# Performance work log

Hardware: AMD Instinct MI355X
Metric: run time of the kernel (lower is better)

The kernel has to match this reference:

```python
import jax, jax.numpy as jnp
import numpy as np

N = 50000
E = 800000
IN_F = 128
OUT_F = 128


def setup_inputs() -> dict:
    key = jax.random.key(0)
    k1, k2, k3, k4, k5 = jax.random.split(key, 5)
    x = jax.random.normal(k1, (N, IN_F), dtype=jnp.float32)
    # sparse adjacency as COO edge list: row = dst (aggregating node), col = src
    edge_index = jax.random.randint(k2, (2, E), 0, N, dtype=jnp.int64)
    edge_weight = jax.random.uniform(k3, (E,), dtype=jnp.float32)
    # nn.Linear(in_features, out_features): W is [out, in], b is [out]
    W = jax.random.normal(k4, (OUT_F, IN_F), dtype=jnp.float32) * (1.0 / np.sqrt(IN_F))
    b = jax.random.normal(k5, (OUT_F,), dtype=jnp.float32) * 0.01
    return {"x": x, "edge_index": edge_index, "edge_weight": edge_weight, "W": W, "b": b}


def reference(x, edge_index, edge_weight, W, b):
    # hidden = self.linear(x)  -> [N, out]
    hidden = jnp.einsum("ni,oi->no", x, W) + b
    # out = adj @ hidden (SpMM): out[dst] += w_e * hidden[src]
    dst = edge_index[0]
    src = edge_index[1]
    msgs = edge_weight[:, None] * hidden[src]  # [E, out]
    out = jax.ops.segment_sum(msgs, dst, num_segments=x.shape[0])
    return out
```

## Files before the change

kernel.cpp:

```cpp
#include <hip/hip_runtime.h>
#include <hip/hip_bf16.h>

#define N_NODES 50000
#define N_EDGES 800000
#define FEAT    128
#define N_TILES (N_NODES / 16)
#define GEMM_BLOCKS 784
#define MAXD    32
#define OVF_CAP 16384
#define NODES_PER_GRP 6250
#define CHUNK   2048
#define NCHUNK  ((N_EDGES + CHUNK - 1) / CHUNK)
#define QCAP    110000
#define SCAT_BPG 98

using short8  = __attribute__((ext_vector_type(8))) short;
using float4v = __attribute__((ext_vector_type(4))) float;


__device__ __forceinline__ unsigned short f2b(float f) {
    __hip_bfloat16 h = __float2bfloat16(f);
    return __builtin_bit_cast(unsigned short, h);
}

__global__ __launch_bounds__(256) void k_prep(const float* __restrict__ W,
                                              int* __restrict__ ws_ints,
                                              unsigned short* __restrict__ wbf) {
    const int gid = blockIdx.x * 256 + threadIdx.x;
    if (gid < 12576) ((int4*)ws_ints)[gid] = make_int4(0, 0, 0, 0);
    if (gid < 2048) {
        const float* s = W + (size_t)gid * 8;
        float4v a0 = *(const float4v*)(s);
        float4v a1 = *(const float4v*)(s + 4);
        short8 v;
        #pragma unroll
        for (int j = 0; j < 4; ++j) { v[j] = (short)f2b(a0[j]); v[4 + j] = (short)f2b(a1[j]); }
        *(short8*)(wbf + (size_t)gid * 8) = v;
    }
}

__global__ __launch_bounds__(256) void k_fused(const float* __restrict__ x,
                                               const unsigned short* __restrict__ wbf,
                                               const float* __restrict__ bias,
                                               unsigned short* __restrict__ hidden,
                                               const int* __restrict__ ei,
                                               const float* __restrict__ wt,
                                               int* __restrict__ flag,
                                               int2* __restrict__ queue) {
    __shared__ int pshared[16];
    const int t = threadIdx.x;

    if (blockIdx.x < GEMM_BLOCKS) {
        const int wave = t >> 6;
        const int lane = t & 63;
        int tile = blockIdx.x * 4 + wave;
        if (tile >= N_TILES) tile = N_TILES - 1;
        const int rowBase = tile * 16;
        const int m    = lane & 15;
        const int quad = lane >> 4;

        float4v acc[8];
        #pragma unroll
        for (int i = 0; i < 8; ++i) acc[i] = (float4v){0.f, 0.f, 0.f, 0.f};

        short8 af[4];
        #pragma unroll
        for (int kk = 0; kk < 4; ++kk) {
            const int k0 = kk * 32 + quad * 8;
            const float* ap = x + (size_t)(rowBase + m) * FEAT + k0;
            float4v a0 = *(const float4v*)(ap);
            float4v a1 = *(const float4v*)(ap + 4);
            #pragma unroll
            for (int j = 0; j < 4; ++j) { af[kk][j] = (short)f2b(a0[j]); af[kk][4 + j] = (short)f2b(a1[j]); }
        }

        #pragma unroll
        for (int nt = 0; nt < 8; ++nt) {
            const unsigned short* wrow = wbf + (size_t)(nt * 16 + m) * FEAT + quad * 8;
            #pragma unroll
            for (int kk = 0; kk < 4; ++kk) {
                short8 bf = *(const short8*)(wrow + kk * 32);
                acc[nt] = __builtin_amdgcn_mfma_f32_16x16x32_bf16(af[kk], bf, acc[nt], 0, 0, 0);
            }
        }

        const int r0 = rowBase + quad * 4;
        #pragma unroll
        for (int nt = 0; nt < 8; ++nt) {
            const int col = nt * 16 + m;
            const float bc = bias[col];
            #pragma unroll
            for (int r = 0; r < 4; ++r) {
                hidden[(size_t)(r0 + r) * FEAT + col] = f2b(acc[nt][r] + bc);
            }
        }
    } else {
        int* lcnt  = pshared;
        int* gbase = pshared + 8;
        const int bid  = blockIdx.x - GEMM_BLOCKS;
        const int lane = t & 63;

        unsigned long long mball = __ballot(ei[2 * lane + 1] != 0);
        const int sh = (mball == 0ULL) ? 1 : 0;

        if (t < 8) lcnt[t] = 0;
        __syncthreads();

        const int e0 = bid * CHUNK + t;
        int      dstv[8];
        unsigned recv_[8];
        int      lpos[8];
        #pragma unroll
        for (int i = 0; i < 8; ++i) {
            int e = e0 + i * 256;
            if (e < N_EDGES) {
                int dst = ei[(size_t)e << sh];
                if ((unsigned)dst >= N_NODES) dst = 0;
                int src = ei[(size_t)(N_EDGES + e) << sh];
                if ((unsigned)src >= N_NODES) src = 0;
                dstv[i]  = dst;
                recv_[i] = ((unsigned)f2b(wt[e]) << 16) | (unsigned)src;
                lpos[i]  = atomicAdd(&lcnt[dst / NODES_PER_GRP], 1);
            } else {
                dstv[i] = -1;
            }
        }
        __syncthreads();
        if (t < 8) gbase[t] = atomicAdd(&flag[16 + 16 * t], lcnt[t]);
        __syncthreads();

        #pragma unroll
        for (int i = 0; i < 8; ++i) {
            if (dstv[i] < 0) continue;
            int g   = dstv[i] / NODES_PER_GRP;
            int idx = gbase[g] + lpos[i];
            if (idx < QCAP) {
                int2 r; r.x = dstv[i]; r.y = (int)recv_[i];
                queue[(size_t)g * QCAP + idx] = r;
            }
        }
    }
}

__global__ __launch_bounds__(256) void k_scat(const int2* __restrict__ queue,
                                              int* __restrict__ flag,
                                              int* __restrict__ fill,
                                              unsigned int* __restrict__ slots,
                                              int2* __restrict__ ovf) {
    const int g = blockIdx.x & 7;
    const int b = blockIdx.x >> 3;
    int n = flag[16 + 16 * g]; if (n > QCAP) n = QCAP;
    const int2* q = queue + (size_t)g * QCAP;

    for (int i = b * 256 + (int)threadIdx.x; i < n; i += SCAT_BPG * 256) {
        int2 ent = q[i];
        int dst = ent.x;
        int pos = atomicAdd(&fill[dst], 1);
        if (pos < MAXD) {
            slots[(size_t)dst * MAXD + pos] = (unsigned int)ent.y;
        } else {
            int op = atomicAdd(&flag[1], 1);
            if (op < OVF_CAP) { int2 r; r.x = dst; r.y = ent.y; ovf[op] = r; }
        }
    }
}

#define AGG_FMA(w_, h_)                                                      \
    acc[0] = fmaf(w_, __uint_as_float((h_.x & 0xffffu) << 16), acc[0]);      \
    acc[1] = fmaf(w_, __uint_as_float(h_.x & 0xffff0000u),     acc[1]);      \
    acc[2] = fmaf(w_, __uint_as_float((h_.y & 0xffffu) << 16), acc[2]);      \
    acc[3] = fmaf(w_, __uint_as_float(h_.y & 0xffff0000u),     acc[3]);      \
    acc[4] = fmaf(w_, __uint_as_float((h_.z & 0xffffu) << 16), acc[4]);      \
    acc[5] = fmaf(w_, __uint_as_float(h_.z & 0xffff0000u),     acc[5]);      \
    acc[6] = fmaf(w_, __uint_as_float((h_.w & 0xffffu) << 16), acc[6]);      \
    acc[7] = fmaf(w_, __uint_as_float(h_.w & 0xffff0000u),     acc[7]);

__global__ __launch_bounds__(256) void k_agg(const int* __restrict__ fill,
                                             const unsigned int* __restrict__ slots,
                                             const unsigned int* __restrict__ hid,
                                             const int* __restrict__ flag,
                                             const int2* __restrict__ ovf,
                                             float* __restrict__ out) {
    const int wave = threadIdx.x >> 6;
    const int lane = threadIdx.x & 63;
    const int node = blockIdx.x * 4 + wave;
    const int grp  = lane >> 4;
    const int sub  = lane & 15;

    const int degf = fill[node];
    const int deg  = (degf > MAXD) ? MAXD : degf;
    const uint4* sl4 = (const uint4*)(slots + (size_t)node * MAXD);

    float acc[8];
    #pragma unroll
    for (int j = 0; j < 8; ++j) acc[j] = 0.f;

    const int iters = (deg + 3) >> 2;
    for (int it = 0; it < iters; it += 4) {
        uint4 r0 = sl4[it];
        uint4 r1 = sl4[(it + 1) & 7];
        uint4 r2 = sl4[(it + 2) & 7];
        uint4 r3 = sl4[(it + 3) & 7];
        unsigned rc0 = (grp < 2) ? (grp == 0 ? r0.x : r0.y) : (grp == 2 ? r0.z : r0.w);
        unsigned rc1 = (grp < 2) ? (grp == 0 ? r1.x : r1.y) : (grp == 2 ? r1.z : r1.w);
        unsigned rc2 = (grp < 2) ? (grp == 0 ? r2.x : r2.y) : (grp == 2 ? r2.z : r2.w);
        unsigned rc3 = (grp < 2) ? (grp == 0 ? r3.x : r3.y) : (grp == 2 ? r3.z : r3.w);
        const int e0 = it * 4 + grp;
        const bool v0 = (e0)      < deg;
        const bool v1 = (e0 + 4)  < deg;
        const bool v2 = (e0 + 8)  < deg;
        const bool v3 = (e0 + 12) < deg;
        const float w0 = v0 ? __uint_as_float(rc0 & 0xffff0000u) : 0.f;
        const float w1 = v1 ? __uint_as_float(rc1 & 0xffff0000u) : 0.f;
        const float w2 = v2 ? __uint_as_float(rc2 & 0xffff0000u) : 0.f;
        const float w3 = v3 ? __uint_as_float(rc3 & 0xffff0000u) : 0.f;
        const unsigned s0 = v0 ? (rc0 & 0xffffu) : 0u;
        const unsigned s1 = v1 ? (rc1 & 0xffffu) : 0u;
        const unsigned s2 = v2 ? (rc2 & 0xffffu) : 0u;
        const unsigned s3 = v3 ? (rc3 & 0xffffu) : 0u;
        uint4 h0 = *((const uint4*)(hid + (size_t)s0 * 64) + sub);
        uint4 h1 = *((const uint4*)(hid + (size_t)s1 * 64) + sub);
        uint4 h2 = *((const uint4*)(hid + (size_t)s2 * 64) + sub);
        uint4 h3 = *((const uint4*)(hid + (size_t)s3 * 64) + sub);
        AGG_FMA(w0, h0)
        AGG_FMA(w1, h1)
        AGG_FMA(w2, h2)
        AGG_FMA(w3, h3)
    }

    if (degf > MAXD) {
        int n = flag[1]; if (n > OVF_CAP) n = OVF_CAP;
        for (int i = 0; i < n; ++i) {
            int2 r = ovf[i];
            if (r.x != node || (i & 3) != grp) continue;
            unsigned rec = (unsigned)r.y;
            float w = __uint_as_float(rec & 0xffff0000u);
            unsigned src = rec & 0xffffu;
            uint4 h = *((const uint4*)(hid + (size_t)src * 64) + sub);
            AGG_FMA(w, h)
        }
    }

    #pragma unroll
    for (int j = 0; j < 8; ++j) {
        float a = acc[j];
        a += __shfl_xor(a, 16, 64);
        a += __shfl_xor(a, 32, 64);
        acc[j] = a;
    }

    if (lane < 16) {
        float* o = out + (size_t)node * FEAT + sub * 8;
        *(float4*)(o)     = make_float4(acc[0], acc[1], acc[2], acc[3]);
        *(float4*)(o + 4) = make_float4(acc[4], acc[5], acc[6], acc[7]);
    }
}

extern "C" void kernel_launch(void* const* d_in, const int* in_sizes, int n_in,
                              void* d_out, int out_size, void* d_ws, size_t ws_size,
                              hipStream_t stream) {
    const float* x  = (const float*)d_in[0];
    const int*   ei = (const int*)d_in[1];
    const float* ew = (const float*)d_in[2];
    const float* W  = (const float*)d_in[3];
    const float* b  = (const float*)d_in[4];
    float* out = (float*)d_out;

    int*  flag = (int*)d_ws;
    int*  fill = flag + 256;
    int2* ovf  = (int2*)(fill + 50048);
    unsigned int* slots = (unsigned int*)(ovf + OVF_CAP);
    unsigned short* hidden = (unsigned short*)(slots + (size_t)N_NODES * MAXD);
    int2* queue = (int2*)(hidden + (size_t)N_NODES * FEAT);
    unsigned short* wbf = (unsigned short*)(queue + (size_t)8 * QCAP);

    k_prep <<<64, 256, 0, stream>>>(W, flag, wbf);
    k_fused<<<GEMM_BLOCKS + NCHUNK, 256, 0, stream>>>(x, wbf, b, hidden, ei, ew,
                                                      flag, queue);
    k_scat <<<8 * SCAT_BPG, 256, 0, stream>>>(queue, flag, fill, slots, ovf);
    k_agg  <<<N_NODES / 4, 256, 0, stream>>>(fill, slots, (const unsigned int*)hidden,
                                             flag, ovf, out);
}
```

Before: 178.2 us.

## Stage swizzled bf16 W in LDS for GEMM and batch scatter atomics

The prep kernel now writes the bf16 weight matrix in an XOR-swizzled layout. Each GEMM block copies the whole matrix into a 32KB shared-memory buffer and reads B fragments from LDS without bank conflicts, instead of reloading them from global memory per wave. The scatter kernel is unrolled by four so several queue loads and fill atomics are in flight at once. The large shared allocation now also applies to the partition blocks, which may lower occupancy there. The added LDS staging and barrier could also cost more than the cached global reads saved.

```diff
diff --git a/kernel.cpp b/kernel.cpp
--- a/kernel.cpp
+++ b/kernel.cpp
@@ -29,13 +29,16 @@
     const int gid = blockIdx.x * 256 + threadIdx.x;
     if (gid < 12576) ((int4*)ws_ints)[gid] = make_int4(0, 0, 0, 0);
     if (gid < 2048) {
-        const float* s = W + (size_t)gid * 8;
+        const int r  = gid >> 4;
+        const int cc = gid & 15;
+        const float* s = W + (size_t)r * FEAT + cc * 8;
         float4v a0 = *(const float4v*)(s);
         float4v a1 = *(const float4v*)(s + 4);
         short8 v;
         #pragma unroll
         for (int j = 0; j < 4; ++j) { v[j] = (short)f2b(a0[j]); v[4 + j] = (short)f2b(a1[j]); }
-        *(short8*)(wbf + (size_t)gid * 8) = v;
+        const int dst = r * 16 + (cc ^ (r & 7));
+        *(short8*)(wbf + (size_t)dst * 8) = v;
     }
 }
 
@@ -47,10 +50,17 @@
                                                const float* __restrict__ wt,
                                                int* __restrict__ flag,
                                                int2* __restrict__ queue) {
-    __shared__ int pshared[16];
+    __shared__ __align__(16) unsigned short Wlds[128 * 128];
     const int t = threadIdx.x;
 
     if (blockIdx.x < GEMM_BLOCKS) {
+        #pragma unroll
+        for (int j = 0; j < 8; ++j) {
+            const int c16 = j * 256 + t;
+            *(short8*)&Wlds[c16 * 8] = *(const short8*)(wbf + (size_t)c16 * 8);
+        }
+        __syncthreads();
+
         const int wave = t >> 6;
         const int lane = t & 63;
         int tile = blockIdx.x * 4 + wave;
@@ -63,24 +73,21 @@
         #pragma unroll
         for (int i = 0; i < 8; ++i) acc[i] = (float4v){0.f, 0.f, 0.f, 0.f};
 
-        short8 af[4];
         #pragma unroll
         for (int kk = 0; kk < 4; ++kk) {
             const int k0 = kk * 32 + quad * 8;
             const float* ap = x + (size_t)(rowBase + m) * FEAT + k0;
             float4v a0 = *(const float4v*)(ap);
             float4v a1 = *(const float4v*)(ap + 4);
+            short8 af;
             #pragma unroll
-            for (int j = 0; j < 4; ++j) { af[kk][j] = (short)f2b(a0[j]); af[kk][4 + j] = (short)f2b(a1[j]); }
-        }
-
-        #pragma unroll
-        for (int nt = 0; nt < 8; ++nt) {
-            const unsigned short* wrow = wbf + (size_t)(nt * 16 + m) * FEAT + quad * 8;
+            for (int j = 0; j < 4; ++j) { af[j] = (short)f2b(a0[j]); af[4 + j] = (short)f2b(a1[j]); }
+            const int cc = kk * 4 + quad;
             #pragma unroll
-            for (int kk = 0; kk < 4; ++kk) {
-                short8 bf = *(const short8*)(wrow + kk * 32);
-                acc[nt] = __builtin_amdgcn_mfma_f32_16x16x32_bf16(af[kk], bf, acc[nt], 0, 0, 0);
+            for (int nt = 0; nt < 8; ++nt) {
+                const int rr = nt * 16 + m;
+                short8 bf = *(const short8*)&Wlds[rr * 128 + ((cc ^ (rr & 7)) << 3)];
+                acc[nt] = __builtin_amdgcn_mfma_f32_16x16x32_bf16(af, bf, acc[nt], 0, 0, 0);
             }
         }
 
@@ -95,8 +102,8 @@
             }
         }
     } else {
-        int* lcnt  = pshared;
-        int* gbase = pshared + 8;
+        int* lcnt  = (int*)Wlds;
+        int* gbase = lcnt + 8;
         const int bid  = blockIdx.x - GEMM_BLOCKS;
         const int lane = t & 63;
 
@@ -151,17 +158,32 @@
     const int b = blockIdx.x >> 3;
     int n = flag[16 + 16 * g]; if (n > QCAP) n = QCAP;
     const int2* q = queue + (size_t)g * QCAP;
-
-    for (int i = b * 256 + (int)threadIdx.x; i < n; i += SCAT_BPG * 256) {
+    const int stride = SCAT_BPG * 256;
+
+    int i = b * 256 + (int)threadIdx.x;
+    for (; i + 3 * stride < n; i += 4 * stride) {
+        int2 e0 = q[i];
+        int2 e1 = q[i + stride];
+        int2 e2 = q[i + 2 * stride];
+        int2 e3 = q[i + 3 * stride];
+        int p0 = atomicAdd(&fill[e0.x], 1);
+        int p1 = atomicAdd(&fill[e1.x], 1);
+        int p2 = atomicAdd(&fill[e2.x], 1);
+        int p3 = atomicAdd(&fill[e3.x], 1);
+        if (p0 < MAXD) slots[(size_t)e0.x * MAXD + p0] = (unsigned)e0.y;
+        else { int op = atomicAdd(&flag[1], 1); if (op < OVF_CAP) ovf[op] = e0; }
+        if (p1 < MAXD) slots[(size_t)e1.x * MAXD + p1] = (unsigned)e1.y;
+        else { int op = atomicAdd(&flag[1], 1); if (op < OVF_CAP) ovf[op] = e1; }
+        if (p2 < MAXD) slots[(size_t)e2.x * MAXD + p2] = (unsigned)e2.y;
+        else { int op = atomicAdd(&flag[1], 1); if (op < OVF_CAP) ovf[op] = e2; }
+        if (p3 < MAXD) slots[(size_t)e3.x * MAXD + p3] = (unsigned)e3.y;
+        else { int op = atomicAdd(&flag[1], 1); if (op < OVF_CAP) ovf[op] = e3; }
+    }
+    for (; i < n; i += stride) {
         int2 ent = q[i];
-        int dst = ent.x;
-        int pos = atomicAdd(&fill[dst], 1);
-        if (pos < MAXD) {
-            slots[(size_t)dst * MAXD + pos] = (unsigned int)ent.y;
-        } else {
-            int op = atomicAdd(&flag[1], 1);
-            if (op < OVF_CAP) { int2 r; r.x = dst; r.y = ent.y; ovf[op] = r; }
-        }
+        int pos = atomicAdd(&fill[ent.x], 1);
+        if (pos < MAXD) slots[(size_t)ent.x * MAXD + pos] = (unsigned)ent.y;
+        else { int op = atomicAdd(&flag[1], 1); if (op < OVF_CAP) ovf[op] = ent; }
     }
 }
 
```

After: 166.9 us. 1.07x faster.
